# Kernel optimization log

Measured on AMD Instinct MI355X. Metric: run time of the kernel, lower is better.

The kernel has to match this reference:

```python
import jax, jax.numpy as jnp
import numpy as np

G, W, H1, H2, H3 = 512, 64, 128, 128, 64
B = 1024

def setup_inputs() -> dict:
    key = jax.random.key(0)
    k0, k1, k2, k3 = jax.random.split(key, 4)
    inputs = jax.random.normal(k0, (B, G * W), dtype=jnp.float32)
    # Glorot-uniform-like scaled init for stacked per-SKU weights
    def glorot(k, shape):
        fan_in, fan_out = shape[-2], shape[-1]
        lim = jnp.sqrt(6.0 / (fan_in + fan_out)).astype(jnp.float32)
        return jax.random.uniform(k, shape, jnp.float32, -lim, lim)
    W1 = glorot(k1, (G, W, H1))
    W2 = glorot(k2, (G, H1, H2))
    W3 = glorot(k3, (G, H2, H3))
    return {"inputs": inputs, "W1": W1, "W2": W2, "W3": W3}

def reference(inputs, W1, W2, W3):
    # inputs: [B, G*W]  -> per-SKU blocks [B, G, W] (SKU-major slicing in original)
    b = inputs.shape[0]
    x = inputs.reshape(b, G, W)
    # Grouped (batched-over-SKU) GEMM + relu per layer; no dropout (training=None)
    x = jax.nn.relu(jnp.einsum('bgw,gwh->bgh', x, W1))  # [B, G, H1]
    x = jax.nn.relu(jnp.einsum('bgh,ghk->bgk', x, W2))  # [B, G, H2]
    x = jax.nn.relu(jnp.einsum('bgk,gko->bgo', x, W3))  # [B, G, H3]
    # concat of per-SKU outputs along axis 1 == SKU-major reshape
    return x.reshape(b, G * H3)
```

## Files before the change

### kernel.cpp

```cpp
#include <hip/hip_runtime.h>

#define NG  512
#define GW  32768
#define GH3 32768

typedef __attribute__((ext_vector_type(8))) short bf16x8;
typedef __attribute__((ext_vector_type(4))) float f32x4;
typedef __attribute__((ext_vector_type(4))) unsigned int u32x4;
typedef __attribute__((ext_vector_type(2))) __bf16 bf16x2;

union frag_u { u32x4 u; bf16x8 h; };

#define MFMA __builtin_amdgcn_mfma_f32_16x16x32_bf16

__device__ __forceinline__ unsigned cvt2bf(float a, float b) {
  bf16x2 v = {(__bf16)a, (__bf16)b};
  return __builtin_bit_cast(unsigned, v);
}

__device__ __forceinline__ void permswap(unsigned &e, unsigned &o) {
  asm volatile("s_nop 1\n\t"
               "v_permlane32_swap_b32 %0, %1\n\t"
               "s_nop 1\n\t"
               "v_permlane16_swap_b32 %0, %1\n\t"
               "s_nop 1"
               : "+v"(e), "+v"(o));
}

__device__ __forceinline__ void mk_bfrag1(f32x4 e, f32x4 o, frag_u &bf) {
  unsigned E0 = cvt2bf(fmaxf(e[0], 0.f), fmaxf(e[1], 0.f));
  unsigned E1 = cvt2bf(fmaxf(e[2], 0.f), fmaxf(e[3], 0.f));
  unsigned O0 = cvt2bf(fmaxf(o[0], 0.f), fmaxf(o[1], 0.f));
  unsigned O1 = cvt2bf(fmaxf(o[2], 0.f), fmaxf(o[3], 0.f));
  permswap(E0, O0);
  permswap(E1, O1);
  bf.u = (u32x4){E0, E1, O0, O1};
}

template<int K, int H>
__device__ __forceinline__ void stage_frag(const float* __restrict__ gsrc,
                                           char* ldsBase, int tid) {
  constexpr int KC = K / 32;
  constexpr int NELEM = (K / 8) * H;
  #pragma unroll
  for (int lin = tid; lin < NELEM; lin += 512) {
    const int h  = lin & (H - 1);
    const int kb = lin / H;
    const float* p = gsrc + h + (size_t)(8 * kb) * H;
    unsigned w0 = cvt2bf(p[0 * H], p[1 * H]);
    unsigned w1 = cvt2bf(p[2 * H], p[3 * H]);
    unsigned w2 = cvt2bf(p[4 * H], p[5 * H]);
    unsigned w3 = cvt2bf(p[6 * H], p[7 * H]);
    const int mt = h >> 4, bl = h & 15, kc = kb >> 2, bq = kb & 3;
    const int byteoff = ((mt * KC + kc) * 64 + bq * 16 + bl) * 16;
    *(u32x4*)(ldsBase + byteoff) = (u32x4){w0, w1, w2, w3};
  }
}

__device__ __forceinline__ void ld_b1(const float* px, frag_u* b1) {
  #pragma unroll
  for (int kc = 0; kc < 2; ++kc) {
    f32x4 lo = *(const f32x4*)(px + 32 * kc);
    f32x4 hi = *(const f32x4*)(px + 32 * kc + 4);
    b1[kc].u = (u32x4){cvt2bf(lo[0], lo[1]), cvt2bf(lo[2], lo[3]),
                       cvt2bf(hi[0], hi[1]), cvt2bf(hi[2], hi[3])};
  }
}

__global__ __launch_bounds__(512, 4)
void DeepBlockDense_kernel(const float* __restrict__ x,
                           const float* __restrict__ w1,
                           const float* __restrict__ w2,
                           const float* __restrict__ w3,
                           float* __restrict__ out) {
  __shared__ __align__(16) char smem[65536];
  const int g    = blockIdx.x;
  const int tid  = threadIdx.x;
  const int lane = tid & 63;
  const int wid  = tid >> 6;
  const int bq   = lane >> 4;

  stage_frag<64 , 128>(w1 + (size_t)g * (64 * 128) , smem        , tid);
  stage_frag<128, 128>(w2 + (size_t)g * (128 * 128), smem + 16384, tid);
  stage_frag<128, 64 >(w3 + (size_t)g * (128 * 64) , smem + 49152, tid);
  __syncthreads();

  const char* aBase = smem + lane * 16;

  #pragma unroll 1
  for (int t = 0; t < 4; ++t) {
    const size_t r0 = (size_t)(t * 256 + wid * 16 + (lane & 15));
    const size_t r1 = r0 + 128;

    frag_u b1a[2], b1b[2];
    ld_b1(x + r0 * GW + g * 64 + 8 * bq, b1a);
    ld_b1(x + r1 * GW + g * 64 + 8 * bq, b1b);

    frag_u b2a[4], b2b[4];
    #pragma unroll
    for (int pr = 0; pr < 4; ++pr) {
      f32x4 ea = {}, oa = {}, eb = {}, ob = {};
      #pragma unroll
      for (int kc = 0; kc < 2; ++kc) {
        frag_u ae, ao;
        ae.u = *(const u32x4*)(aBase + 1024 * ((2 * pr    ) * 2 + kc));
        ao.u = *(const u32x4*)(aBase + 1024 * ((2 * pr + 1) * 2 + kc));
        ea = MFMA(ae.h, b1a[kc].h, ea, 0, 0, 0);
        eb = MFMA(ae.h, b1b[kc].h, eb, 0, 0, 0);
        oa = MFMA(ao.h, b1a[kc].h, oa, 0, 0, 0);
        ob = MFMA(ao.h, b1b[kc].h, ob, 0, 0, 0);
      }
      mk_bfrag1(ea, oa, b2a[pr]);
      mk_bfrag1(eb, ob, b2b[pr]);
    }

    f32x4 acc3a[4] = {}, acc3b[4] = {};
    #pragma unroll
    for (int pr = 0; pr < 4; ++pr) {
      f32x4 ea = {}, oa = {}, eb = {}, ob = {};
      #pragma unroll
      for (int kc = 0; kc < 4; ++kc) {
        frag_u ae, ao;
        ae.u = *(const u32x4*)(aBase + 16384 + 1024 * ((2 * pr    ) * 4 + kc));
        ao.u = *(const u32x4*)(aBase + 16384 + 1024 * ((2 * pr + 1) * 4 + kc));
        ea = MFMA(ae.h, b2a[kc].h, ea, 0, 0, 0);
        eb = MFMA(ae.h, b2b[kc].h, eb, 0, 0, 0);
        oa = MFMA(ao.h, b2a[kc].h, oa, 0, 0, 0);
        ob = MFMA(ao.h, b2b[kc].h, ob, 0, 0, 0);
      }
      frag_u b3a, b3b;
      mk_bfrag1(ea, oa, b3a);
      mk_bfrag1(eb, ob, b3b);
      #pragma unroll
      for (int mt = 0; mt < 4; ++mt) {
        frag_u a;
        a.u = *(const u32x4*)(aBase + 49152 + 1024 * (mt * 4 + pr));
        acc3a[mt] = MFMA(a.h, b3a.h, acc3a[mt], 0, 0, 0);
        acc3b[mt] = MFMA(a.h, b3b.h, acc3b[mt], 0, 0, 0);
      }
    }

    float* po0 = out + r0 * GH3 + g * 64 + 4 * bq;
    float* po1 = out + r1 * GH3 + g * 64 + 4 * bq;
    #pragma unroll
    for (int mt = 0; mt < 4; ++mt) {
      f32x4 va = acc3a[mt], vb = acc3b[mt];
      va[0] = fmaxf(va[0], 0.f); va[1] = fmaxf(va[1], 0.f);
      va[2] = fmaxf(va[2], 0.f); va[3] = fmaxf(va[3], 0.f);
      vb[0] = fmaxf(vb[0], 0.f); vb[1] = fmaxf(vb[1], 0.f);
      vb[2] = fmaxf(vb[2], 0.f); vb[3] = fmaxf(vb[3], 0.f);
      *(f32x4*)(po0 + 16 * mt) = va;
      *(f32x4*)(po1 + 16 * mt) = vb;
    }
  }
}

extern "C" void kernel_launch(void* const* d_in, const int* in_sizes, int n_in,
                              void* d_out, int out_size, void* d_ws, size_t ws_size,
                              hipStream_t stream) {
  const float* x  = (const float*)d_in[0];
  const float* w1 = (const float*)d_in[1];
  const float* w2 = (const float*)d_in[2];
  const float* w3 = (const float*)d_in[3];
  float* out = (float*)d_out;
  (void)in_sizes; (void)n_in; (void)out_size; (void)d_ws; (void)ws_size;
  DeepBlockDense_kernel<<<dim3(NG), dim3(512), 0, stream>>>(x, w1, w2, w3, out);
}
```

Baseline: 85.33 us.

## Prefetch next input tile into registers and raise wave priority during MFMA

After: 88.77 us. +4.0%, slower.

```diff
diff --git a/kernel.cpp b/kernel.cpp
--- a/kernel.cpp
+++ b/kernel.cpp
@@ -57,14 +57,18 @@
   }
 }
 
-__device__ __forceinline__ void ld_b1(const float* px, frag_u* b1) {
-  #pragma unroll
-  for (int kc = 0; kc < 2; ++kc) {
-    f32x4 lo = *(const f32x4*)(px + 32 * kc);
-    f32x4 hi = *(const f32x4*)(px + 32 * kc + 4);
-    b1[kc].u = (u32x4){cvt2bf(lo[0], lo[1]), cvt2bf(lo[2], lo[3]),
-                       cvt2bf(hi[0], hi[1]), cvt2bf(hi[2], hi[3])};
-  }
+__device__ __forceinline__ void ld_raw(const float* px, f32x4* d) {
+  d[0] = *(const f32x4*)(px + 0);
+  d[1] = *(const f32x4*)(px + 4);
+  d[2] = *(const f32x4*)(px + 32);
+  d[3] = *(const f32x4*)(px + 36);
+}
+
+__device__ __forceinline__ void cvt_b1(const f32x4* d, frag_u* b1) {
+  b1[0].u = (u32x4){cvt2bf(d[0][0], d[0][1]), cvt2bf(d[0][2], d[0][3]),
+                    cvt2bf(d[1][0], d[1][1]), cvt2bf(d[1][2], d[1][3])};
+  b1[1].u = (u32x4){cvt2bf(d[2][0], d[2][1]), cvt2bf(d[2][2], d[2][3]),
+                    cvt2bf(d[3][0], d[3][1]), cvt2bf(d[3][2], d[3][3])};
 }
 
 __global__ __launch_bounds__(512, 4)
@@ -80,6 +84,12 @@
   const int wid  = tid >> 6;
   const int bq   = lane >> 4;
 
+  const float* xbase = x + g * 64 + 8 * bq + (size_t)(wid * 16 + (lane & 15)) * GW;
+
+  f32x4 xra[4], xrb[4];
+  ld_raw(xbase + (size_t)0   * GW, xra);
+  ld_raw(xbase + (size_t)128 * GW, xrb);
+
   stage_frag<64 , 128>(w1 + (size_t)g * (64 * 128) , smem        , tid);
   stage_frag<128, 128>(w2 + (size_t)g * (128 * 128), smem + 16384, tid);
   stage_frag<128, 64 >(w3 + (size_t)g * (128 * 64) , smem + 49152, tid);
@@ -93,8 +103,14 @@
     const size_t r1 = r0 + 128;
 
     frag_u b1a[2], b1b[2];
-    ld_b1(x + r0 * GW + g * 64 + 8 * bq, b1a);
-    ld_b1(x + r1 * GW + g * 64 + 8 * bq, b1b);
+    cvt_b1(xra, b1a);
+    cvt_b1(xrb, b1b);
+    if (t < 3) {
+      ld_raw(xbase + (size_t)(t * 256 + 256) * GW, xra);
+      ld_raw(xbase + (size_t)(t * 256 + 384) * GW, xrb);
+    }
+
+    __builtin_amdgcn_s_setprio(1);
 
     frag_u b2a[4], b2b[4];
     #pragma unroll
@@ -140,6 +156,8 @@
       }
     }
 
+    __builtin_amdgcn_s_setprio(0);
+
     float* po0 = out + r0 * GH3 + g * 64 + 4 * bq;
     float* po1 = out + r1 * GH3 + g * 64 + 4 * bq;
     #pragma unroll
```
